# Optimization experiments

Hardware: AMD Instinct MI355X
Metric: run time of the kernel (lower is better)

## Reference

```python
import jax
import jax.numpy as jnp
import numpy as np

SIGMA = 0.5
COLLISION_WEIGHT = 100.0
CE_WEIGHTS = (1.0, 30.0, 30.0, 10.0)
B, V, F, P = 512, 778, 1538, 1024


def _cone_field(tri, pts):
    # Conical distance field of receiver triangle `tri` [B,P,3,3] evaluated at
    # intruder vertices `pts` [B,P,3,3] (Tzionas et al. penetration field,
    # penalize_outside=False, point2plane=False). Returns [B,P].
    c = tri.mean(axis=-2)                                   # triangle center [B,P,3]
    n = jnp.cross(tri[..., 1, :] - tri[..., 0, :], tri[..., 2, :] - tri[..., 0, :])
    n = n / (jnp.linalg.norm(n, axis=-1, keepdims=True) + 1e-9)
    d = pts - c[..., None, :]                               # [B,P,3,3]
    h = jnp.einsum('bpvc,bpc->bpv', d, n)                   # signed height along normal
    rho2 = jnp.maximum(jnp.sum(d * d, axis=-1) - h * h, 0.0)  # squared radial dist
    phi = jax.nn.relu(-h) * jnp.exp(-rho2 / (2.0 * SIGMA * SIGMA))
    return phi.sum(axis=-1)


def _pen_distance(triangles, collision_idxs):
    # triangles [B,2F,3,3]; collision_idxs [B,P,2] with -1 padding -> per-batch loss [B]
    bb = jnp.arange(triangles.shape[0])[:, None]
    valid = (collision_idxs[..., 0] >= 0) & (collision_idxs[..., 1] >= 0)
    idx = jnp.maximum(collision_idxs, 0)
    recv = triangles[bb, idx[..., 0]]                       # [B,P,3,3]
    intr = triangles[bb, idx[..., 1]]
    pair = _cone_field(recv, intr) + _cone_field(intr, recv)
    return jnp.sum(pair * valid, axis=1)


def _collision_loss(out_vertices, faces, collision_idxs):
    nv = out_vertices.shape[2]
    verts = jnp.concatenate([out_vertices[0], out_vertices[1]], axis=1)   # [B,2V,3]
    faces_comb = jnp.concatenate([faces[0], faces[1] + nv], axis=0)       # [2F,3]
    triangles = verts[:, faces_comb]                                      # [B,2F,3,3]
    loss_b = _pen_distance(triangles, collision_idxs)
    nz = (loss_b != 0).astype(loss_b.dtype)
    cnt = nz.sum()
    return jnp.where(cnt > 0, (loss_b * nz).sum() / jnp.maximum(cnt, 1.0) * COLLISION_WEIGHT, 0.0)


def _index_loss(elem, mask):
    # masked mean exactly as Loss.index_losss: sum(loss*mask)/ (mask.sum()*D), 0 if empty
    l = elem.reshape(elem.shape[0], -1)
    denom = mask.sum() * l.shape[1]
    return jnp.where(denom > 0, (l * mask[:, None]).sum() / jnp.maximum(denom, 1.0), 0.0)


def _mse(a, b):
    return (a - b) ** 2


def _l1(a, b):
    return jnp.abs(a - b)


def setup_inputs():
    key = jax.random.key(0)
    ks = jax.random.split(key, 20)
    f32 = jnp.float32
    out_vertices = jax.random.normal(ks[0], (2, B, V, 3), f32) * 0.05
    out_betas = jax.random.normal(ks[1], (2, B, 10), f32)
    out_transl = jax.random.normal(ks[2], (2, B, 3), f32) * 0.1
    out_j3d = jax.random.normal(ks[3], (2, B, 21, 3), f32) * 0.1
    out_go = jax.random.normal(ks[4], (2, B, 3), f32)
    out_pose = jax.random.normal(ks[5], (2, B, 45), f32)
    tgt_trans = jax.random.normal(ks[6], (2, B, 3), f32) * 0.1
    tgt_j3d = jax.random.normal(ks[7], (2, B, 21, 3), f32) * 0.1
    tgt_go = jax.random.normal(ks[8], (2, B, 3), f32)
    tgt_pose = jax.random.normal(ks[9], (2, B, 45), f32)
    tgt_shape = jax.random.normal(ks[10], (2, B, 10), f32)
    class_logits = jax.random.normal(ks[11], (B, 4), f32)
    faces = jax.random.randint(ks[12], (2, F, 3), 0, V, jnp.int32)
    ci = jax.random.randint(ks[13], (B, P, 2), 0, 2 * F, jnp.int32)
    keep = jax.random.uniform(ks[14], (B, P, 1)) < 0.7
    collision_idxs = jnp.where(keep, ci, -1)
    handedness = jax.random.randint(ks[15], (B, 2), 0, 2, jnp.int32)
    valid = jax.random.randint(ks[16], (2, B), 0, 2, jnp.int32)
    class_targets = jax.random.randint(ks[17], (B,), 0, 4, jnp.int32)
    return dict(out_vertices=out_vertices, out_betas=out_betas, out_transl=out_transl,
                out_j3d=out_j3d, out_go=out_go, out_pose=out_pose, tgt_trans=tgt_trans,
                tgt_j3d=tgt_j3d, tgt_go=tgt_go, tgt_pose=tgt_pose, tgt_shape=tgt_shape,
                class_logits=class_logits, faces=faces, collision_idxs=collision_idxs,
                handedness=handedness, valid=valid, class_targets=class_targets)


def reference(out_vertices, out_betas, out_transl, out_j3d, out_go, out_pose,
              tgt_trans, tgt_j3d, tgt_go, tgt_pose, tgt_shape, class_logits,
              faces, collision_idxs, handedness, valid, class_targets):
    f32 = out_vertices.dtype
    loss_interpen = _collision_loss(out_vertices, faces, collision_idxs)
    inter = (handedness.sum(axis=1) == 2).astype(f32)
    loss_inter_shape = _index_loss(_mse(out_betas[0], out_betas[1]), inter)
    loss_inter_transl = _index_loss(_mse(out_transl[0] - out_transl[1],
                                         tgt_trans[0] - tgt_trans[1]), inter) * 100.0
    loss_inter_j3d = _index_loss(_mse(out_j3d[0] - out_j3d[1],
                                      tgt_j3d[0] - tgt_j3d[1]), inter) * 100.0
    lgo = lhp = lrj = lj3 = lsh = ltr = reg = jnp.zeros((), f32)
    for h in range(2):  # left, right
        m = valid[h].astype(f32)
        lgo = lgo + _index_loss(_mse(out_go[h], tgt_go[h]), m) * 10.0
        lhp = lhp + _index_loss(_mse(out_pose[h], tgt_pose[h]), m) * 10.0
        lrj = lrj + _index_loss(_l1((out_j3d[h][:, 1:] - out_j3d[h][:, :1]) * 1000.0,
                                    (tgt_j3d[h][:, 1:] - tgt_j3d[h][:, :1]) * 1000.0), m) * 0.01
        lj3 = lj3 + _index_loss(_l1(out_j3d[h] * 1000.0, tgt_j3d[h] * 1000.0), m) * 0.01
        lsh = lsh + _index_loss(_mse(out_betas[h], tgt_shape[h]), m) * 10.0
        ltr = ltr + _index_loss(_l1(out_transl[h], tgt_trans[h]), m) * 10.0
        reg = reg + 0.1 * _index_loss(_mse(out_betas[h], out_betas[h]), m)
        reg = reg + _index_loss(_mse(out_pose[h], out_pose[h]), m)
    # weighted cross entropy with ignore_index=0 (torch semantics)
    logp = jax.nn.log_softmax(class_logits, axis=-1)
    nll = -jnp.take_along_axis(logp, class_targets[:, None], axis=1)[:, 0]
    w = jnp.asarray(CE_WEIGHTS, f32)[class_targets]
    vmask = (class_targets != 0).astype(f32)
    ce = jnp.sum(w * vmask * nll) / jnp.maximum(jnp.sum(w * vmask), 1e-9)
    return jnp.stack([loss_interpen, loss_inter_shape, loss_inter_transl, loss_inter_j3d,
                      lgo, lhp, lrj, lj3, lsh, ltr, reg, ce])
```

## Files before the change

### kernel.cpp

```cpp
#include <hip/hip_runtime.h>
#include <math.h>

#define BB 512
#define VV 778
#define FF 1538
#define PP 1024
#define NS 16

__device__ __forceinline__ float cone3(const float3 t[3], const float3 p[3]) {
    const float third = 1.0f / 3.0f;
    float cx = (t[0].x + t[1].x + t[2].x) * third;
    float cy = (t[0].y + t[1].y + t[2].y) * third;
    float cz = (t[0].z + t[1].z + t[2].z) * third;
    float e1x = t[1].x - t[0].x, e1y = t[1].y - t[0].y, e1z = t[1].z - t[0].z;
    float e2x = t[2].x - t[0].x, e2y = t[2].y - t[0].y, e2z = t[2].z - t[0].z;
    float nx = e1y * e2z - e1z * e2y;
    float ny = e1z * e2x - e1x * e2z;
    float nz = e1x * e2y - e1y * e2x;
    float inv = 1.0f / (sqrtf(nx * nx + ny * ny + nz * nz) + 1e-9f);
    nx *= inv; ny *= inv; nz *= inv;
    float s = 0.0f;
#pragma unroll
    for (int i = 0; i < 3; i++) {
        float dx = p[i].x - cx, dy = p[i].y - cy, dz = p[i].z - cz;
        float h = dx * nx + dy * ny + dz * nz;
        float r2 = fmaxf(dx * dx + dy * dy + dz * dz - h * h, 0.0f);
        float rl = fmaxf(-h, 0.0f);
        s += rl * expf(-2.0f * r2);
    }
    return s;
}

__device__ __forceinline__ void loadTri(const int* __restrict__ faces,
                                        const float* __restrict__ sv,
                                        int f, float3 t[3]) {
    int off = (f >= FF) ? (VV * 3) : 0;
    const int* fp = faces + f * 3;
#pragma unroll
    for (int k = 0; k < 3; k++) {
        int j = fp[k] * 3 + off;
        t[k] = make_float3(sv[j], sv[j + 1], sv[j + 2]);
    }
}

__global__ __launch_bounds__(256) void per_batch_kernel(
    const float* __restrict__ verts,
    const int*   __restrict__ faces,
    const int*   __restrict__ cidx,
    const float* __restrict__ betas,
    const float* __restrict__ transl,
    const float* __restrict__ j3d,
    const float* __restrict__ go,
    const float* __restrict__ pose,
    const float* __restrict__ tgt_trans,
    const float* __restrict__ tgt_j3d,
    const float* __restrict__ tgt_go,
    const float* __restrict__ tgt_pose,
    const float* __restrict__ tgt_shape,
    float* __restrict__ ws)
{
    __shared__ float sv[2 * VV * 3];
    __shared__ float red[4][NS];
    const int b = blockIdx.x, tid = threadIdx.x;

    const float* v0 = verts + (size_t)b * VV * 3;
    const float* v1 = verts + (size_t)(BB + b) * VV * 3;
    for (int i = tid; i < VV * 3; i += 256) {
        sv[i] = v0[i];
        sv[VV * 3 + i] = v1[i];
    }
    __syncthreads();

    float part[NS];
#pragma unroll
    for (int k = 0; k < NS; k++) part[k] = 0.0f;

    const int2* ci = (const int2*)cidx + (size_t)b * PP;
    for (int p = tid; p < PP; p += 256) {
        int2 fp = ci[p];
        if (fp.x < 0 || fp.y < 0) continue;
        float3 r[3], q[3];
        loadTri(faces, sv, fp.x, r);
        loadTri(faces, sv, fp.y, q);
        part[0] += cone3(r, q) + cone3(q, r);
    }

    if (tid < 63) {
        const int t = tid;
        if (t < 10) { float d = betas[b * 10 + t] - betas[(BB + b) * 10 + t]; part[1] = d * d; }
        if (t < 3) {
            float d = (transl[b * 3 + t] - transl[(BB + b) * 3 + t]) -
                      (tgt_trans[b * 3 + t] - tgt_trans[(BB + b) * 3 + t]);
            part[2] = d * d;
        }
        {
            float d = (j3d[b * 63 + t] - j3d[(BB + b) * 63 + t]) -
                      (tgt_j3d[b * 63 + t] - tgt_j3d[(BB + b) * 63 + t]);
            part[3] = d * d;
        }
#pragma unroll
        for (int h = 0; h < 2; h++) {
            const int base = 4 + 6 * h;
            const size_t ob = (size_t)(h * BB + b);
            if (t < 3)  { float d = go[ob * 3 + t] - tgt_go[ob * 3 + t]; part[base + 0] = d * d; }
            if (t < 45) { float d = pose[ob * 45 + t] - tgt_pose[ob * 45 + t]; part[base + 1] = d * d; }
            if (t < 60) {
                int j = 1 + t / 3, c = t % 3;
                float a  = (j3d[ob * 63 + j * 3 + c]     - j3d[ob * 63 + c]) * 1000.0f;
                float b2 = (tgt_j3d[ob * 63 + j * 3 + c] - tgt_j3d[ob * 63 + c]) * 1000.0f;
                part[base + 2] = fabsf(a - b2);
            }
            {
                float a = j3d[ob * 63 + t] * 1000.0f, b2 = tgt_j3d[ob * 63 + t] * 1000.0f;
                part[base + 3] = fabsf(a - b2);
            }
            if (t < 10) { float d = betas[ob * 10 + t] - tgt_shape[ob * 10 + t]; part[base + 4] = d * d; }
            if (t < 3)  { float d = transl[ob * 3 + t] - tgt_trans[ob * 3 + t]; part[base + 5] = fabsf(d); }
        }
    }

#pragma unroll
    for (int off = 32; off >= 1; off >>= 1) {
#pragma unroll
        for (int k = 0; k < NS; k++) part[k] += __shfl_down(part[k], off);
    }
    const int wave = tid >> 6, lane = tid & 63;
    if (lane == 0) {
#pragma unroll
        for (int k = 0; k < NS; k++) red[wave][k] = part[k];
    }
    __syncthreads();
    if (tid < NS) {
        ws[b * NS + tid] = red[0][tid] + red[1][tid] + red[2][tid] + red[3][tid];
    }
}

__global__ __launch_bounds__(256) void finalize_kernel(
    const float* __restrict__ ws,
    const int*   __restrict__ handed,
    const int*   __restrict__ validm,
    const float* __restrict__ logits,
    const int*   __restrict__ ctgt,
    float* __restrict__ out)
{
    const int tid = threadIdx.x;
    const int NA = 22;
    float acc[22];
#pragma unroll
    for (int k = 0; k < NA; k++) acc[k] = 0.0f;

    for (int b = tid; b < BB; b += 256) {
        const float* w = ws + b * NS;
        float lb = w[0];
        acc[0] += lb;
        acc[1] += (lb != 0.0f) ? 1.0f : 0.0f;
        float inter = ((handed[b * 2] + handed[b * 2 + 1]) == 2) ? 1.0f : 0.0f;
        acc[2] += inter * w[1];
        acc[3] += inter * w[2];
        acc[4] += inter * w[3];
        acc[5] += inter;
#pragma unroll
        for (int h = 0; h < 2; h++) {
            float vm = (float)validm[h * BB + b];
            const int ab = 6 + 7 * h;
#pragma unroll
            for (int k = 0; k < 6; k++) acc[ab + k] += vm * w[4 + 6 * h + k];
            acc[ab + 6] += vm;
        }
        float l0 = logits[b * 4 + 0], l1 = logits[b * 4 + 1];
        float l2 = logits[b * 4 + 2], l3 = logits[b * 4 + 3];
        float m = fmaxf(fmaxf(l0, l1), fmaxf(l2, l3));
        float lse = m + logf(expf(l0 - m) + expf(l1 - m) + expf(l2 - m) + expf(l3 - m));
        int t = ctgt[b];
        float lt = (t == 0) ? l0 : (t == 1) ? l1 : (t == 2) ? l2 : l3;
        float nll = lse - lt;
        float cw = (t == 0) ? 1.0f : (t == 3) ? 10.0f : 30.0f;
        float vm = (t != 0) ? 1.0f : 0.0f;
        acc[20] += cw * vm * nll;
        acc[21] += cw * vm;
    }

#pragma unroll
    for (int off = 32; off >= 1; off >>= 1) {
#pragma unroll
        for (int k = 0; k < NA; k++) acc[k] += __shfl_down(acc[k], off);
    }
    __shared__ float red[4][22];
    const int wave = tid >> 6, lane = tid & 63;
    if (lane == 0) {
#pragma unroll
        for (int k = 0; k < NA; k++) red[wave][k] = acc[k];
    }
    __syncthreads();

    if (tid == 0) {
        float s[22];
#pragma unroll
        for (int k = 0; k < NA; k++)
            s[k] = red[0][k] + red[1][k] + red[2][k] + red[3][k];

        auto idxloss = [](float num, float cnt, float K) -> float {
            float denom = cnt * K;
            return (denom > 0.0f) ? num / fmaxf(denom, 1.0f) : 0.0f;
        };

        out[0] = (s[1] > 0.0f) ? s[0] / fmaxf(s[1], 1.0f) * 100.0f : 0.0f;
        out[1] = idxloss(s[2], s[5], 10.0f);
        out[2] = idxloss(s[3], s[5], 3.0f) * 100.0f;
        out[3] = idxloss(s[4], s[5], 63.0f) * 100.0f;
        out[4] = (idxloss(s[6],  s[12], 3.0f)  + idxloss(s[13], s[19], 3.0f))  * 10.0f;
        out[5] = (idxloss(s[7],  s[12], 45.0f) + idxloss(s[14], s[19], 45.0f)) * 10.0f;
        out[6] = (idxloss(s[8],  s[12], 60.0f) + idxloss(s[15], s[19], 60.0f)) * 0.01f;
        out[7] = (idxloss(s[9],  s[12], 63.0f) + idxloss(s[16], s[19], 63.0f)) * 0.01f;
        out[8] = (idxloss(s[10], s[12], 10.0f) + idxloss(s[17], s[19], 10.0f)) * 10.0f;
        out[9] = (idxloss(s[11], s[12], 3.0f)  + idxloss(s[18], s[19], 3.0f))  * 10.0f;
        out[10] = 0.0f;
        out[11] = s[20] / fmaxf(s[21], 1e-9f);
    }
}

extern "C" void kernel_launch(void* const* d_in, const int* in_sizes, int n_in,
                              void* d_out, int out_size, void* d_ws, size_t ws_size,
                              hipStream_t stream) {
    const float* verts   = (const float*)d_in[0];
    const float* betas   = (const float*)d_in[1];
    const float* transl  = (const float*)d_in[2];
    const float* j3d     = (const float*)d_in[3];
    const float* go      = (const float*)d_in[4];
    const float* pose    = (const float*)d_in[5];
    const float* tt      = (const float*)d_in[6];
    const float* tj      = (const float*)d_in[7];
    const float* tg      = (const float*)d_in[8];
    const float* tp      = (const float*)d_in[9];
    const float* tsh     = (const float*)d_in[10];
    const float* logits  = (const float*)d_in[11];
    const int*   faces   = (const int*)d_in[12];
    const int*   cidx    = (const int*)d_in[13];
    const int*   handed  = (const int*)d_in[14];
    const int*   validm  = (const int*)d_in[15];
    const int*   ctgt    = (const int*)d_in[16];
    float*       ws      = (float*)d_ws;
    float*       out     = (float*)d_out;

    per_batch_kernel<<<BB, 256, 0, stream>>>(verts, faces, cidx, betas, transl,
                                             j3d, go, pose, tt, tj, tg, tp, tsh, ws);
    finalize_kernel<<<1, 256, 0, stream>>>(ws, handed, validm, logits, ctgt, out);
}
```

Measured before the change: 108.3 us.

## Stage faces in LDS, pad vertices to float4, and use 512-thread blocks

Vertices are now stored in shared memory as padded float4 so each corner is one vector LDS read. The whole combined face table (about 37 KB) is also copied into shared memory, so the index lookups no longer go to global memory. The block size doubles to 512 threads, giving each thread fewer collision pairs. The trade-off is that every block copies the full face table, and the larger LDS footprint (about 62 KB) limits how many blocks fit per CU.

```diff
diff --git a/kernel.cpp b/kernel.cpp
--- a/kernel.cpp
+++ b/kernel.cpp
@@ -6,6 +6,7 @@
 #define FF 1538
 #define PP 1024
 #define NS 16
+#define TPB 512
 
 __device__ __forceinline__ float cone3(const float3 t[3], const float3 p[3]) {
     const float third = 1.0f / 3.0f;
@@ -31,19 +32,7 @@
     return s;
 }
 
-__device__ __forceinline__ void loadTri(const int* __restrict__ faces,
-                                        const float* __restrict__ sv,
-                                        int f, float3 t[3]) {
-    int off = (f >= FF) ? (VV * 3) : 0;
-    const int* fp = faces + f * 3;
-#pragma unroll
-    for (int k = 0; k < 3; k++) {
-        int j = fp[k] * 3 + off;
-        t[k] = make_float3(sv[j], sv[j + 1], sv[j + 2]);
-    }
-}
-
-__global__ __launch_bounds__(256) void per_batch_kernel(
+__global__ __launch_bounds__(TPB) void per_batch_kernel(
     const float* __restrict__ verts,
     const int*   __restrict__ faces,
     const int*   __restrict__ cidx,
@@ -59,16 +48,20 @@
     const float* __restrict__ tgt_shape,
     float* __restrict__ ws)
 {
-    __shared__ float sv[2 * VV * 3];
-    __shared__ float red[4][NS];
+    __shared__ float4 sv4[2 * VV];
+    __shared__ int    sfc[2 * FF * 3];
+    __shared__ float  red[TPB / 64][NS];
     const int b = blockIdx.x, tid = threadIdx.x;
 
     const float* v0 = verts + (size_t)b * VV * 3;
     const float* v1 = verts + (size_t)(BB + b) * VV * 3;
-    for (int i = tid; i < VV * 3; i += 256) {
-        sv[i] = v0[i];
-        sv[VV * 3 + i] = v1[i];
-    }
+    float* svf = (float*)sv4;
+    for (int i = tid; i < VV * 3; i += TPB) {
+        int v = i / 3, c = i - v * 3;
+        svf[(v << 2) + c]          = v0[i];
+        svf[((VV + v) << 2) + c]   = v1[i];
+    }
+    for (int i = tid; i < 2 * FF * 3; i += TPB) sfc[i] = faces[i];
     __syncthreads();
 
     float part[NS];
@@ -76,12 +69,28 @@
     for (int k = 0; k < NS; k++) part[k] = 0.0f;
 
     const int2* ci = (const int2*)cidx + (size_t)b * PP;
-    for (int p = tid; p < PP; p += 256) {
+    for (int p = tid; p < PP; p += TPB) {
         int2 fp = ci[p];
         if (fp.x < 0 || fp.y < 0) continue;
         float3 r[3], q[3];
-        loadTri(faces, sv, fp.x, r);
-        loadTri(faces, sv, fp.y, q);
+        {
+            int off = (fp.x >= FF) ? VV : 0;
+            const int* f = sfc + fp.x * 3;
+#pragma unroll
+            for (int k = 0; k < 3; k++) {
+                float4 w = sv4[f[k] + off];
+                r[k] = make_float3(w.x, w.y, w.z);
+            }
+        }
+        {
+            int off = (fp.y >= FF) ? VV : 0;
+            const int* f = sfc + fp.y * 3;
+#pragma unroll
+            for (int k = 0; k < 3; k++) {
+                float4 w = sv4[f[k] + off];
+                q[k] = make_float3(w.x, w.y, w.z);
+            }
+        }
         part[0] += cone3(r, q) + cone3(q, r);
     }
 
@@ -131,7 +140,10 @@
     }
     __syncthreads();
     if (tid < NS) {
-        ws[b * NS + tid] = red[0][tid] + red[1][tid] + red[2][tid] + red[3][tid];
+        float s = 0.0f;
+#pragma unroll
+        for (int w = 0; w < TPB / 64; w++) s += red[w][tid];
+        ws[b * NS + tid] = s;
     }
 }
 
@@ -242,7 +254,7 @@
     float*       ws      = (float*)d_ws;
     float*       out     = (float*)d_out;
 
-    per_batch_kernel<<<BB, 256, 0, stream>>>(verts, faces, cidx, betas, transl,
+    per_batch_kernel<<<BB, TPB, 0, stream>>>(verts, faces, cidx, betas, transl,
                                              j3d, go, pose, tt, tj, tg, tp, tsh, ws);
     finalize_kernel<<<1, 256, 0, stream>>>(ws, handed, validm, logits, ctgt, out);
 }
```

Result: no change. 106.9 us (-1.3%).
